# Optimization experiments

Measured on AMD Instinct MI355X. Metric: run time of the kernel, lower is better.

Reference implementation:

```python
import jax, jax.numpy as jnp
import numpy as np

B, T, D, H = 32, 512, 1024, 1024  # batch, seq, input_size, hidden_size


def _xavier(key, shape):
    fan_in, fan_out = shape
    limit = float(np.sqrt(6.0 / (fan_in + fan_out)))
    return jax.random.uniform(key, shape, jnp.float32, -limit, limit)


def setup_inputs() -> dict:
    key = jax.random.key(0)
    k1, k2, k3 = jax.random.split(key, 3)
    x = jax.random.normal(k1, (B, T, D), jnp.float32)
    weight_ih = _xavier(k2, (D, 4 * H))
    weight_hh = _xavier(k3, (H, 4 * H))
    bias = jnp.zeros((4 * H,), jnp.float32)
    return {"x": x, "weight_ih": weight_ih, "weight_hh": weight_hh, "bias": bias}


def _lstm(x, weight_ih, weight_hh, bias):
    HS = weight_hh.shape[0]
    bs = x.shape[0]
    # Precompute input projections for all timesteps in one big GEMM.
    x_proj = jnp.einsum('btd,dg->btg', x, weight_ih) + bias  # [B,T,4H]
    h0 = jnp.zeros((bs, HS), x.dtype)
    c0 = jnp.zeros((bs, HS), x.dtype)

    def step(carry, xp_t):
        h, c = carry
        gates = xp_t + h @ weight_hh  # [B,4H]
        i_t = jax.nn.sigmoid(gates[:, :HS])
        f_t = jax.nn.sigmoid(gates[:, HS:2 * HS])
        g_t = jnp.tanh(gates[:, 2 * HS:3 * HS])
        o_t = jax.nn.sigmoid(gates[:, 3 * HS:])
        c = f_t * c + i_t * g_t
        h = o_t * jnp.tanh(c)
        return (h, c), h

    (h_T, c_T), hs = jax.lax.scan(step, (h0, c0), jnp.swapaxes(x_proj, 0, 1))
    hidden_seq = jnp.swapaxes(hs, 0, 1)  # [B,T,H]
    return hidden_seq, (h_T, c_T)


def reference(x, weight_ih, weight_hh, bias):
    return _lstm(x, weight_ih, weight_hh, bias)
```

## Files before the change

### kernel.cpp

```cpp
#include <hip/hip_runtime.h>

typedef unsigned short ushort_t;
typedef unsigned int   uint32;
typedef unsigned long long ull_t;
typedef __attribute__((ext_vector_type(8))) short short8;
typedef __attribute__((ext_vector_type(4))) float floatx4;

#define B_    32
#define T_    512
#define H_    1024
#define G4_   4096
#define HSEQ_ (B_*T_*H_)

#define NBLK 64

#define XPROJ_OFF 0ul
#define WTIH_OFF  134217728ul
#define WTHH_OFF  142606336ul
#define H0X_OFF   150994944ul
#define H1X_OFF   151060480ul
#define FLAGS_OFF 151126016ul
#define WS_NEED   151130112ul

#define H0_OFF  0ul
#define H1_OFF  65536ul
#define CTR_OFF 131072ul

__device__ __forceinline__ ushort_t f2b_rne(float f) {
    uint32 u = __float_as_uint(f);
    u += 0x7fffu + ((u >> 16) & 1u);
    return (ushort_t)(u >> 16);
}
__device__ __forceinline__ float b2f(ushort_t u) { return __uint_as_float(((uint32)u) << 16); }
__device__ __forceinline__ float sigm(float x)  { return 1.f / (1.f + __expf(-x)); }
__device__ __forceinline__ float tanh_(float x) { return 1.f - 2.f / (__expf(2.f * x) + 1.f); }

__global__ void transpose_cvt2(const float* __restrict__ in0, ushort_t* __restrict__ out0,
                               const float* __restrict__ in1, ushort_t* __restrict__ out1)
{
    const int gb = blockIdx.x;
    const float*    in  = (gb < 2048) ? in0  : in1;
    ushort_t*       out = (gb < 2048) ? out0 : out1;
    const int id = (gb & 2047) * 256 + threadIdx.x;
    const int n  = id & 4095;
    const int k0 = (id >> 12) * 8;
    union { ushort_t v[8]; uint4 q; } r;
#pragma unroll
    for (int j = 0; j < 8; j++)
        r.v[j] = f2b_rne(in[(size_t)(k0 + j) * G4_ + n]);
    *(uint4*)(out + (size_t)n * 1024 + k0) = r.q;
}

__launch_bounds__(256, 2)
__global__ void gemm_xproj(const float* __restrict__ A, const ushort_t* __restrict__ Bt,
                           const float* __restrict__ bias, ushort_t* __restrict__ C)
{
    __shared__ ushort_t As[128 * 32];
    __shared__ ushort_t Bs[128 * 32];
    const int tid = threadIdx.x;
    const int wave = tid >> 6, lane = tid & 63, l16 = lane & 15, quad = lane >> 4;
    const int wm = (wave >> 1) * 64, wn = (wave & 1) * 64;
    const int m0 = blockIdx.y * 128, n0 = blockIdx.x * 128;
    const int r = tid >> 2;
    const int kp = (tid & 3) * 8;

    floatx4 acc[4][4];
#pragma unroll
    for (int i = 0; i < 4; i++)
#pragma unroll
        for (int j = 0; j < 4; j++) acc[i][j] = (floatx4){0.f, 0.f, 0.f, 0.f};

    for (int kk = 0; kk < 1024; kk += 32) {
#pragma unroll
        for (int h = 0; h < 2; h++) {
            const float* ap = A + (size_t)(m0 + r + h * 64) * 1024 + kk + kp;
            const uint4 u0 = *(const uint4*)ap;
            const uint4 u1 = *(const uint4*)(ap + 4);
            uint4 p;
            p.x = __builtin_amdgcn_perm(u0.y, u0.x, 0x07060302u);
            p.y = __builtin_amdgcn_perm(u0.w, u0.z, 0x07060302u);
            p.z = __builtin_amdgcn_perm(u1.y, u1.x, 0x07060302u);
            p.w = __builtin_amdgcn_perm(u1.w, u1.z, 0x07060302u);
            *(uint4*)&As[(r + h * 64) * 32 + kp] = p;
        }
        const ushort_t* bp = Bt + (size_t)(n0 + r) * 1024 + kk + kp;
        *(uint4*)&Bs[r * 32 + kp]        = *(const uint4*)bp;
        *(uint4*)&Bs[(r + 64) * 32 + kp] = *(const uint4*)(bp + 64 * 1024);
        __syncthreads();

        short8 af[4], bfr[4];
#pragma unroll
        for (int i = 0; i < 4; i++) af[i]  = *(const short8*)&As[(wm + i * 16 + l16) * 32 + quad * 8];
#pragma unroll
        for (int j = 0; j < 4; j++) bfr[j] = *(const short8*)&Bs[(wn + j * 16 + l16) * 32 + quad * 8];
#pragma unroll
        for (int i = 0; i < 4; i++)
#pragma unroll
            for (int j = 0; j < 4; j++)
                acc[i][j] = __builtin_amdgcn_mfma_f32_16x16x32_bf16(af[i], bfr[j], acc[i][j], 0, 0, 0);
        __syncthreads();
    }

#pragma unroll
    for (int i = 0; i < 4; i++) {
        const int gm = m0 + wm + i * 16 + quad * 4;
#pragma unroll
        for (int j = 0; j < 4; j++) {
            const int gn = n0 + wn + j * 16 + l16;
            const float bv = bias[gn];
#pragma unroll
            for (int rr = 0; rr < 4; rr++)
                C[(size_t)(gm + rr) * G4_ + gn] = f2b_rne(acc[i][j][rr] + bv);
        }
    }
}

__launch_bounds__(512, 2)
__global__ void lstm_scan_xp(const ushort_t* __restrict__ xproj,
                             const ushort_t* __restrict__ wthh,
                             ushort_t* __restrict__ h0buf,
                             ushort_t* __restrict__ h1buf,
                             float* __restrict__ out,
                             uint32* __restrict__ flags)
{
    const int tid  = threadIdx.x;
    const int bid  = blockIdx.x;
    const int wave = tid >> 6, lane = tid & 63, l16 = lane & 15, quad = lane >> 4;
    const int g     = wave & 3;
    const int khalf = wave >> 2;
    const int unit0 = bid * 16;
    const int col0  = g * 1024 + unit0 + l16;

    __shared__ ushort_t hs[32 * 1024];
    __shared__ float gA[4 * 32 * 17];
    __shared__ float gB[4 * 32 * 17];
    __shared__ uint32 cnt;

    short8 whf[16];
#pragma unroll
    for (int kk = 0; kk < 16; kk++)
        whf[kk] = *(const short8*)(wthh + (size_t)col0 * 1024 + khalf * 512 + kk * 32 + quad * 8);

    if (tid == 0) cnt = 0;

    const int eb = tid >> 4, ej = tid & 15;
    const int hwoff = (bid >> 1) * 1024 + eb * 32 + 16 * (bid & 1) + ej;
    float cst = 0.f;

    const int b0 = l16, b1 = l16 + 16;
    const int off0 = (b0 * 64 + quad * 16) ^ ((b0 & 7) << 4);
    const int off1 = (b1 * 64 + quad * 16) ^ ((b1 & 7) << 4);
    const int rowbase = khalf * 16 * 2048;

    const int src0  = wave * 8;
    const int abase = (lane >> 1) * 64 + (lane & 1) * 16;

    ushort_t xq[4];
    {
        const ushort_t* xp = xproj + ((size_t)eb * T_ + 0) * G4_ + unit0 + ej;
#pragma unroll
        for (int gg = 0; gg < 4; gg++) xq[gg] = xp[gg * 1024];
    }

    __syncthreads();

    for (int t = 0; t < 512; t++) {
        const ushort_t* hr = (t & 1) ? h1buf : h0buf;
        ushort_t*       hw = (t & 1) ? h0buf : h1buf;

        for (;;) {
            int rdy = 1;
            if (lane < 8)
                rdy = (__hip_atomic_load(&flags[(src0 + lane) * 16],
                                         __ATOMIC_RELAXED, __HIP_MEMORY_SCOPE_AGENT)
                       >= (uint32)t);
            if (__ballot(rdy) == ~0ull) break;
        }

        {
            ull_t d0[8], d1[8];
#pragma unroll
            for (int sl = 0; sl < 8; sl++) {
                const int S = src0 + sl;
                const size_t a = (size_t)(S >> 1) * 2048 + (size_t)((S & 1) * 32 + abase);
                const char* p = (const char*)hr + a;
                d0[sl] = __hip_atomic_load((const ull_t*)p,
                                           __ATOMIC_RELAXED, __HIP_MEMORY_SCOPE_AGENT);
                d1[sl] = __hip_atomic_load((const ull_t*)(p + 8),
                                           __ATOMIC_RELAXED, __HIP_MEMORY_SCOPE_AGENT);
            }
#pragma unroll
            for (int sl = 0; sl < 8; sl++) {
                const int S = src0 + sl;
                const int c = ((S >> 1) * 2048 + (S & 1) * 32 + abase) >> 4;
                const int dst = (c * 16) ^ (((c >> 2) & 7) << 4);
                uint4 v;
                *(ull_t*)&v.x = d0[sl];
                *(ull_t*)&v.z = d1[sl];
                *(uint4*)((char*)hs + dst) = v;
            }
        }
        __syncthreads();

        floatx4 a0a = (floatx4){0.f, 0.f, 0.f, 0.f};
        floatx4 a0b = a0a, a1a = a0a, a1b = a0a;
#pragma unroll
        for (int kk = 0; kk < 16; kk++) {
            const char* base = (const char*)hs + rowbase + kk * 2048;
            const short8 a0 = *(const short8*)(base + off0);
            const short8 a1 = *(const short8*)(base + off1);
            if (kk & 1) {
                a0b = __builtin_amdgcn_mfma_f32_16x16x32_bf16(a0, whf[kk], a0b, 0, 0, 0);
                a1b = __builtin_amdgcn_mfma_f32_16x16x32_bf16(a1, whf[kk], a1b, 0, 0, 0);
            } else {
                a0a = __builtin_amdgcn_mfma_f32_16x16x32_bf16(a0, whf[kk], a0a, 0, 0, 0);
                a1a = __builtin_amdgcn_mfma_f32_16x16x32_bf16(a1, whf[kk], a1a, 0, 0, 0);
            }
        }
        const floatx4 s0 = a0a + a0b;
        const floatx4 s1 = a1a + a1b;
        float* gd = khalf ? gB : gA;
#pragma unroll
        for (int rr = 0; rr < 4; rr++) {
            gd[(g * 32 + quad * 4 + rr) * 17 + l16]      = s0[rr];
            gd[(g * 32 + 16 + quad * 4 + rr) * 17 + l16] = s1[rr];
        }
        __syncthreads();

        float hval, cval;
        {
            const float gi = gA[(0 * 32 + eb) * 17 + ej] + gB[(0 * 32 + eb) * 17 + ej] + b2f(xq[0]);
            const float gf = gA[(1 * 32 + eb) * 17 + ej] + gB[(1 * 32 + eb) * 17 + ej] + b2f(xq[1]);
            const float gg = gA[(2 * 32 + eb) * 17 + ej] + gB[(2 * 32 + eb) * 17 + ej] + b2f(xq[2]);
            const float go = gA[(3 * 32 + eb) * 17 + ej] + gB[(3 * 32 + eb) * 17 + ej] + b2f(xq[3]);
            const float iv = sigm(gi);
            const float fv = sigm(gf);
            const float gv = tanh_(gg);
            const float ov = sigm(go);
            cval = fv * cst + iv * gv;
            cst = cval;
            hval = ov * tanh_(cval);
        }

        {
            const uint32 myb = (uint32)f2b_rne(hval);
            const uint32 nbb = (uint32)__shfl_xor((int)myb, 1);
            if ((ej & 1) == 0)
                __hip_atomic_store((uint32*)(hw + hwoff), myb | (nbb << 16),
                                   __ATOMIC_RELAXED, __HIP_MEMORY_SCOPE_AGENT);
        }

        if (t < 511) {
            asm volatile("s_waitcnt vmcnt(0)" ::: "memory");
            if (lane == 0) {
                const uint32 old = __hip_atomic_fetch_add(&cnt, 1u,
                                       __ATOMIC_RELAXED, __HIP_MEMORY_SCOPE_WORKGROUP);
                if (old == (uint32)(8 * t + 7))
                    __hip_atomic_store(&flags[bid * 16], (uint32)(t + 1),
                                       __ATOMIC_RELAXED, __HIP_MEMORY_SCOPE_AGENT);
            }
            out[((size_t)eb * T_ + t) * H_ + unit0 + ej] = hval;
            {
                const ushort_t* xp = xproj + ((size_t)eb * T_ + (t + 1)) * G4_ + unit0 + ej;
#pragma unroll
                for (int gg = 0; gg < 4; gg++) xq[gg] = xp[gg * 1024];
            }
        } else {
            out[((size_t)eb * T_ + t) * H_ + unit0 + ej] = hval;
            out[HSEQ_ + eb * H_ + unit0 + ej] = hval;
            out[HSEQ_ + B_ * H_ + eb * H_ + unit0 + ej] = cval;
        }
    }
}

__launch_bounds__(512, 2)
__global__ void lstm_scan_fused(const float* __restrict__ x,
                                const float* __restrict__ wih,
                                const float* __restrict__ whh,
                                const float* __restrict__ bias,
                                ushort_t* __restrict__ h0buf,
                                ushort_t* __restrict__ h1buf,
                                float* __restrict__ out,
                                uint32* __restrict__ ctr)
{
    const int tid  = threadIdx.x;
    const int bid  = blockIdx.x;
    const int wave = tid >> 6, lane = tid & 63, l16 = lane & 15, quad = lane >> 4;
    const int g     = wave & 3;
    const int khalf = wave >> 2;
    const int unit0 = bid * 16;
    const int col0  = g * 1024 + unit0 + l16;
    const int kbase = khalf * 512;

    __shared__ ushort_t xs[32 * 1024];
    __shared__ float gA[4 * 32 * 17];
    __shared__ float gB[4 * 32 * 17];

    short8 wif[16], whf[16];
#pragma unroll
    for (int kk = 0; kk < 16; kk++) {
        short8 vi, vh;
#pragma unroll
        for (int j = 0; j < 8; j++) {
            const size_t k = (size_t)(kbase + kk * 32 + quad * 8 + j);
            vi[j] = (short)f2b_rne(wih[k * G4_ + col0]);
            vh[j] = (short)f2b_rne(whh[k * G4_ + col0]);
        }
        wif[kk] = vi;
        whf[kk] = vh;
    }
    const float bcol = (khalf == 0) ? bias[col0] : 0.f;

    const int eb = tid >> 4, ej = tid & 15;
    const int hwoff = (bid >> 1) * 1024 + eb * 32 + 16 * (bid & 1) + ej;
    float cst = 0.f;

    floatx4 a0a, a0b, a1a, a1b;

    {
        const int sb = tid >> 4, sc = tid & 15;
        const float* xrow = x + ((size_t)sb * T_ + 0) * H_ + sc * 64;
#pragma unroll
        for (int q = 0; q < 8; q++) {
            const uint4 u0 = *(const uint4*)(xrow + q * 8);
            const uint4 u1 = *(const uint4*)(xrow + q * 8 + 4);
            uint4 p;
            p.x = __builtin_amdgcn_perm(u0.y, u0.x, 0x07060302u);
            p.y = __builtin_amdgcn_perm(u0.w, u0.z, 0x07060302u);
            p.z = __builtin_amdgcn_perm(u1.y, u1.x, 0x07060302u);
            p.w = __builtin_amdgcn_perm(u1.w, u1.z, 0x07060302u);
            const int k = sc * 64 + q * 8;
            *(uint4*)&xs[(k >> 5) * 1024 + sb * 32 + (k & 31)] = p;
        }
    }
    __syncthreads();
    a0a = (floatx4){bcol, bcol, bcol, bcol};
    a1a = a0a;
    a0b = (floatx4){0.f, 0.f, 0.f, 0.f};
    a1b = a0b;
#pragma unroll
    for (int kk = 0; kk < 16; kk++) {
        const ushort_t* ps = &xs[(khalf * 16 + kk) * 1024 + quad * 8];
        const short8 a0 = *(const short8*)(ps + l16 * 32);
        const short8 a1 = *(const short8*)(ps + (16 + l16) * 32);
        if (kk & 1) {
            a0b = __builtin_amdgcn_mfma_f32_16x16x32_bf16(a0, wif[kk], a0b, 0, 0, 0);
            a1b = __builtin_amdgcn_mfma_f32_16x16x32_bf16(a1, wif[kk], a1b, 0, 0, 0);
        } else {
            a0a = __builtin_amdgcn_mfma_f32_16x16x32_bf16(a0, wif[kk], a0a, 0, 0, 0);
            a1a = __builtin_amdgcn_mfma_f32_16x16x32_bf16(a1, wif[kk], a1a, 0, 0, 0);
        }
    }

    for (int t = 0; t < 512; t++) {
        const ushort_t* hr = (t & 1) ? h1buf : h0buf;
        ushort_t*       hw = (t & 1) ? h0buf : h1buf;

#pragma unroll
        for (int kk = 0; kk < 16; kk++) {
            const ushort_t* pa = hr + (khalf * 16 + kk) * 1024 + quad * 8;
            const short8 a0 = *(const short8*)(pa + l16 * 32);
            const short8 a1 = *(const short8*)(pa + (16 + l16) * 32);
            if (kk & 1) {
                a0b = __builtin_amdgcn_mfma_f32_16x16x32_bf16(a0, whf[kk], a0b, 0, 0, 0);
                a1b = __builtin_amdgcn_mfma_f32_16x16x32_bf16(a1, whf[kk], a1b, 0, 0, 0);
            } else {
                a0a = __builtin_amdgcn_mfma_f32_16x16x32_bf16(a0, whf[kk], a0a, 0, 0, 0);
                a1a = __builtin_amdgcn_mfma_f32_16x16x32_bf16(a1, whf[kk], a1a, 0, 0, 0);
            }
        }
        const floatx4 s0 = a0a + a0b;
        const floatx4 s1 = a1a + a1b;
        float* gd = khalf ? gB : gA;
#pragma unroll
        for (int rr = 0; rr < 4; rr++) {
            gd[(g * 32 + quad * 4 + rr) * 17 + l16]      = s0[rr];
            gd[(g * 32 + 16 + quad * 4 + rr) * 17 + l16] = s1[rr];
        }
        __syncthreads();

        {
            const float gi = gA[(0 * 32 + eb) * 17 + ej] + gB[(0 * 32 + eb) * 17 + ej];
            const float gf = gA[(1 * 32 + eb) * 17 + ej] + gB[(1 * 32 + eb) * 17 + ej];
            const float gg = gA[(2 * 32 + eb) * 17 + ej] + gB[(2 * 32 + eb) * 17 + ej];
            const float go = gA[(3 * 32 + eb) * 17 + ej] + gB[(3 * 32 + eb) * 17 + ej];
            const float iv = sigm(gi);
            const float fv = sigm(gf);
            const float gv = tanh_(gg);
            const float ov = sigm(go);
            const float c = fv * cst + iv * gv;
            cst = c;
            const float h = ov * tanh_(c);
            hw[hwoff] = f2b_rne(h);
            out[((size_t)eb * T_ + t) * H_ + unit0 + ej] = h;
            if (t == 511) {
                out[HSEQ_ + eb * H_ + unit0 + ej] = h;
                out[HSEQ_ + B_ * H_ + eb * H_ + unit0 + ej] = cst;
            }
        }
        __syncthreads();

        if (t < 511) {
            if (tid == 0) {
                __threadfence();
                __hip_atomic_fetch_add(ctr, 1u, __ATOMIC_RELAXED, __HIP_MEMORY_SCOPE_AGENT);
            }
            {
                const int sb = tid >> 4, sc = tid & 15;
                const float* xrow = x + ((size_t)sb * T_ + (t + 1)) * H_ + sc * 64;
#pragma unroll
                for (int q = 0; q < 8; q++) {
                    const uint4 u0 = *(const uint4*)(xrow + q * 8);
                    const uint4 u1 = *(const uint4*)(xrow + q * 8 + 4);
                    uint4 p;
                    p.x = __builtin_amdgcn_perm(u0.y, u0.x, 0x07060302u);
                    p.y = __builtin_amdgcn_perm(u0.w, u0.z, 0x07060302u);
                    p.z = __builtin_amdgcn_perm(u1.y, u1.x, 0x07060302u);
                    p.w = __builtin_amdgcn_perm(u1.w, u1.z, 0x07060302u);
                    const int k = sc * 64 + q * 8;
                    *(uint4*)&xs[(k >> 5) * 1024 + sb * 32 + (k & 31)] = p;
                }
            }
            __syncthreads();
            a0a = (floatx4){bcol, bcol, bcol, bcol};
            a1a = a0a;
            a0b = (floatx4){0.f, 0.f, 0.f, 0.f};
            a1b = a0b;
#pragma unroll
            for (int kk = 0; kk < 16; kk++) {
                const ushort_t* ps = &xs[(khalf * 16 + kk) * 1024 + quad * 8];
                const short8 a0 = *(const short8*)(ps + l16 * 32);
                const short8 a1 = *(const short8*)(ps + (16 + l16) * 32);
                if (kk & 1) {
                    a0b = __builtin_amdgcn_mfma_f32_16x16x32_bf16(a0, wif[kk], a0b, 0, 0, 0);
                    a1b = __builtin_amdgcn_mfma_f32_16x16x32_bf16(a1, wif[kk], a1b, 0, 0, 0);
                } else {
                    a0a = __builtin_amdgcn_mfma_f32_16x16x32_bf16(a0, wif[kk], a0a, 0, 0, 0);
                    a1a = __builtin_amdgcn_mfma_f32_16x16x32_bf16(a1, wif[kk], a1a, 0, 0, 0);
                }
            }
            if (tid == 0) {
                const uint32 target = (uint32)NBLK * (uint32)(t + 1);
                while (__hip_atomic_load(ctr, __ATOMIC_RELAXED, __HIP_MEMORY_SCOPE_AGENT) < target) {
                    __builtin_amdgcn_s_sleep(1);
                }
                __threadfence();
            }
            __syncthreads();
        }
    }
}

extern "C" void kernel_launch(void* const* d_in, const int* in_sizes, int n_in,
                              void* d_out, int out_size, void* d_ws, size_t ws_size,
                              hipStream_t stream)
{
    const float* x    = (const float*)d_in[0];
    const float* wih  = (const float*)d_in[1];
    const float* whh  = (const float*)d_in[2];
    const float* bias = (const float*)d_in[3];
    float* out = (float*)d_out;
    char* ws = (char*)d_ws;

    if (ws_size >= WS_NEED) {
        ushort_t* xproj = (ushort_t*)(ws + XPROJ_OFF);
        ushort_t* wtih  = (ushort_t*)(ws + WTIH_OFF);
        ushort_t* wthh  = (ushort_t*)(ws + WTHH_OFF);
        ushort_t* h0    = (ushort_t*)(ws + H0X_OFF);
        ushort_t* h1    = (ushort_t*)(ws + H1X_OFF);
        uint32*   flags = (uint32*)(ws + FLAGS_OFF);

        hipMemsetAsync(ws + H0X_OFF, 0, 2 * 65536 + 4096, stream);
        hipLaunchKernelGGL(transpose_cvt2, dim3(4096), dim3(256), 0, stream,
                           wih, wtih, whh, wthh);
        hipLaunchKernelGGL(gemm_xproj, dim3(32, 128), dim3(256), 0, stream,
                           x, wtih, bias, xproj);
        hipLaunchKernelGGL(lstm_scan_xp, dim3(NBLK), dim3(512), 0, stream,
                           xproj, wthh, h0, h1, out, flags);
    } else {
        ushort_t* h0  = (ushort_t*)(ws + H0_OFF);
        ushort_t* h1  = (ushort_t*)(ws + H1_OFF);
        uint32*   ctr = (uint32*)(ws + CTR_OFF);

        hipMemsetAsync(ws, 0, 131072 + 256, stream);
        hipLaunchKernelGGL(lstm_scan_fused, dim3(NBLK), dim3(512), 0, stream,
                           x, wih, whh, bias, h0, h1, out, ctr);
    }
}
```

Measured before the change: 2.567 ms.

## Split batch into two independent planes with separate flags to overlap recurrence sync

The persistent LSTM scan now splits the 32-sequence batch into two 16-row planes. Each plane has its own double-buffered h arrays, completion flags and counters, and the two planes are processed one after the other inside each timestep. The aim is to let one plane's cross-block flag wait and h exchange overlap with the other plane's MFMA and gate work, shortening the critical path of the inter-block synchronization. The cost is twice as many barriers and flag polls per step, and half-sized MFMA batches that use the preloaded weight fragments less efficiently.

```diff
diff --git a/kernel.cpp b/kernel.cpp
--- a/kernel.cpp
+++ b/kernel.cpp
@@ -17,8 +17,10 @@
 #define XPROJ_OFF 0ul
 #define WTIH_OFF  134217728ul
 #define WTHH_OFF  142606336ul
-#define H0X_OFF   150994944ul
-#define H1X_OFF   151060480ul
+#define H0A_OFF   150994944ul
+#define H1A_OFF   (H0A_OFF +  32768ul)
+#define H0B_OFF   (H0A_OFF +  65536ul)
+#define H1B_OFF   (H0A_OFF +  98304ul)
 #define FLAGS_OFF 151126016ul
 #define WS_NEED   151130112ul
 
@@ -118,10 +120,13 @@
 __launch_bounds__(512, 2)
 __global__ void lstm_scan_xp(const ushort_t* __restrict__ xproj,
                              const ushort_t* __restrict__ wthh,
-                             ushort_t* __restrict__ h0buf,
-                             ushort_t* __restrict__ h1buf,
+                             ushort_t* __restrict__ h0A,
+                             ushort_t* __restrict__ h1A,
+                             ushort_t* __restrict__ h0B,
+                             ushort_t* __restrict__ h1B,
                              float* __restrict__ out,
-                             uint32* __restrict__ flags)
+                             uint32* __restrict__ flagsA,
+                             uint32* __restrict__ flagsB)
 {
     const int tid  = threadIdx.x;
     const int bid  = blockIdx.x;
@@ -131,29 +136,30 @@
     const int unit0 = bid * 16;
     const int col0  = g * 1024 + unit0 + l16;
 
-    __shared__ ushort_t hs[32 * 1024];
-    __shared__ float gA[4 * 32 * 17];
-    __shared__ float gB[4 * 32 * 17];
-    __shared__ uint32 cnt;
+    __shared__ ushort_t hs[16 * 1024];
+    __shared__ float gA[4 * 16 * 17];
+    __shared__ float gB[4 * 16 * 17];
+    __shared__ uint32 cntA, cntB;
 
     short8 whf[16];
 #pragma unroll
     for (int kk = 0; kk < 16; kk++)
         whf[kk] = *(const short8*)(wthh + (size_t)col0 * 1024 + khalf * 512 + kk * 32 + quad * 8);
 
-    if (tid == 0) cnt = 0;
-
-    const int eb = tid >> 4, ej = tid & 15;
-    const int hwoff = (bid >> 1) * 1024 + eb * 32 + 16 * (bid & 1) + ej;
+    if (tid == 0) { cntA = 0; cntB = 0; }
+
+    const int eb      = tid >> 4;
+    const int ej      = tid & 15;
+    const int myplane = eb >> 4;
+    const int bloc    = eb & 15;
     float cst = 0.f;
 
-    const int b0 = l16, b1 = l16 + 16;
-    const int off0 = (b0 * 64 + quad * 16) ^ ((b0 & 7) << 4);
-    const int off1 = (b1 * 64 + quad * 16) ^ ((b1 & 7) << 4);
-    const int rowbase = khalf * 16 * 2048;
-
-    const int src0  = wave * 8;
-    const int abase = (lane >> 1) * 64 + (lane & 1) * 16;
+    const int off0    = (l16 * 64 + quad * 16) ^ ((l16 & 7) << 4);
+    const int rowbase = khalf * 16 * 1024;
+
+    const int src0 = wave * 8;
+    const int sb   = lane >> 2;
+    const int part = lane & 3;
 
     ushort_t xq[4];
     {
@@ -165,110 +171,103 @@
     __syncthreads();
 
     for (int t = 0; t < 512; t++) {
-        const ushort_t* hr = (t & 1) ? h1buf : h0buf;
-        ushort_t*       hw = (t & 1) ? h0buf : h1buf;
-
-        for (;;) {
-            int rdy = 1;
-            if (lane < 8)
-                rdy = (__hip_atomic_load(&flags[(src0 + lane) * 16],
-                                         __ATOMIC_RELAXED, __HIP_MEMORY_SCOPE_AGENT)
-                       >= (uint32)t);
-            if (__ballot(rdy) == ~0ull) break;
-        }
-
-        {
-            ull_t d0[8], d1[8];
-#pragma unroll
-            for (int sl = 0; sl < 8; sl++) {
-                const int S = src0 + sl;
-                const size_t a = (size_t)(S >> 1) * 2048 + (size_t)((S & 1) * 32 + abase);
-                const char* p = (const char*)hr + a;
-                d0[sl] = __hip_atomic_load((const ull_t*)p,
+#pragma unroll
+        for (int P = 0; P < 2; P++) {
+            const ushort_t* hr = (P == 0) ? ((t & 1) ? h1A : h0A)
+                                          : ((t & 1) ? h1B : h0B);
+            ushort_t*       hw = (P == 0) ? ((t & 1) ? h0A : h1A)
+                                          : ((t & 1) ? h0B : h1B);
+            uint32*  fl  = (P == 0) ? flagsA : flagsB;
+            uint32*  cp  = (P == 0) ? &cntA : &cntB;
+
+            for (;;) {
+                int rdy = 1;
+                if (lane < 8)
+                    rdy = (__hip_atomic_load(&fl[(src0 + lane) * 8],
+                                             __ATOMIC_RELAXED, __HIP_MEMORY_SCOPE_AGENT)
+                           >= (uint32)t);
+                if (__ballot(rdy) == ~0ull) break;
+            }
+
+            {
+                ull_t d[8];
+#pragma unroll
+                for (int sl = 0; sl < 8; sl++) {
+                    const int S = src0 + sl;
+                    d[sl] = __hip_atomic_load(
+                        (const ull_t*)(hr + (size_t)sb * 1024 + S * 16 + part * 4),
+                        __ATOMIC_RELAXED, __HIP_MEMORY_SCOPE_AGENT);
+                }
+#pragma unroll
+                for (int sl = 0; sl < 8; sl++) {
+                    const int S = src0 + sl;
+                    const int dst = (S >> 1) * 1024 + sb * 64 + (S & 1) * 32 + part * 8;
+                    const int gi  = dst >> 4;
+                    const int swz = ((gi * 16) ^ (((gi >> 2) & 7) << 4)) + (dst & 15);
+                    *(ull_t*)((char*)hs + swz) = d[sl];
+                }
+            }
+            __syncthreads();
+
+            floatx4 aa = (floatx4){0.f, 0.f, 0.f, 0.f};
+            floatx4 ab = aa;
+#pragma unroll
+            for (int kk = 0; kk < 16; kk++) {
+                const char* base = (const char*)hs + rowbase + kk * 1024;
+                const short8 a0 = *(const short8*)(base + off0);
+                if (kk & 1) ab = __builtin_amdgcn_mfma_f32_16x16x32_bf16(a0, whf[kk], ab, 0, 0, 0);
+                else        aa = __builtin_amdgcn_mfma_f32_16x16x32_bf16(a0, whf[kk], aa, 0, 0, 0);
+            }
+            const floatx4 s0 = aa + ab;
+            float* gd = khalf ? gB : gA;
+#pragma unroll
+            for (int rr = 0; rr < 4; rr++)
+                gd[(g * 16 + quad * 4 + rr) * 17 + l16] = s0[rr];
+            __syncthreads();
+
+            if (myplane == P) {
+                const float gi = gA[(0 * 16 + bloc) * 17 + ej] + gB[(0 * 16 + bloc) * 17 + ej] + b2f(xq[0]);
+                const float gf = gA[(1 * 16 + bloc) * 17 + ej] + gB[(1 * 16 + bloc) * 17 + ej] + b2f(xq[1]);
+                const float gg = gA[(2 * 16 + bloc) * 17 + ej] + gB[(2 * 16 + bloc) * 17 + ej] + b2f(xq[2]);
+                const float go = gA[(3 * 16 + bloc) * 17 + ej] + gB[(3 * 16 + bloc) * 17 + ej] + b2f(xq[3]);
+                const float iv = sigm(gi);
+                const float fv = sigm(gf);
+                const float gv = tanh_(gg);
+                const float ov = sigm(go);
+                const float cval = fv * cst + iv * gv;
+                cst = cval;
+                const float hval = ov * tanh_(cval);
+
+                {
+                    const uint32 myb = (uint32)f2b_rne(hval);
+                    const uint32 nbb = (uint32)__shfl_xor((int)myb, 1);
+                    if ((ej & 1) == 0)
+                        __hip_atomic_store((uint32*)(hw + (size_t)bloc * 1024 + unit0 + ej),
+                                           myb | (nbb << 16),
                                            __ATOMIC_RELAXED, __HIP_MEMORY_SCOPE_AGENT);
-                d1[sl] = __hip_atomic_load((const ull_t*)(p + 8),
-                                           __ATOMIC_RELAXED, __HIP_MEMORY_SCOPE_AGENT);
-            }
-#pragma unroll
-            for (int sl = 0; sl < 8; sl++) {
-                const int S = src0 + sl;
-                const int c = ((S >> 1) * 2048 + (S & 1) * 32 + abase) >> 4;
-                const int dst = (c * 16) ^ (((c >> 2) & 7) << 4);
-                uint4 v;
-                *(ull_t*)&v.x = d0[sl];
-                *(ull_t*)&v.z = d1[sl];
-                *(uint4*)((char*)hs + dst) = v;
-            }
-        }
-        __syncthreads();
-
-        floatx4 a0a = (floatx4){0.f, 0.f, 0.f, 0.f};
-        floatx4 a0b = a0a, a1a = a0a, a1b = a0a;
-#pragma unroll
-        for (int kk = 0; kk < 16; kk++) {
-            const char* base = (const char*)hs + rowbase + kk * 2048;
-            const short8 a0 = *(const short8*)(base + off0);
-            const short8 a1 = *(const short8*)(base + off1);
-            if (kk & 1) {
-                a0b = __builtin_amdgcn_mfma_f32_16x16x32_bf16(a0, whf[kk], a0b, 0, 0, 0);
-                a1b = __builtin_amdgcn_mfma_f32_16x16x32_bf16(a1, whf[kk], a1b, 0, 0, 0);
-            } else {
-                a0a = __builtin_amdgcn_mfma_f32_16x16x32_bf16(a0, whf[kk], a0a, 0, 0, 0);
-                a1a = __builtin_amdgcn_mfma_f32_16x16x32_bf16(a1, whf[kk], a1a, 0, 0, 0);
-            }
-        }
-        const floatx4 s0 = a0a + a0b;
-        const floatx4 s1 = a1a + a1b;
-        float* gd = khalf ? gB : gA;
-#pragma unroll
-        for (int rr = 0; rr < 4; rr++) {
-            gd[(g * 32 + quad * 4 + rr) * 17 + l16]      = s0[rr];
-            gd[(g * 32 + 16 + quad * 4 + rr) * 17 + l16] = s1[rr];
-        }
-        __syncthreads();
-
-        float hval, cval;
-        {
-            const float gi = gA[(0 * 32 + eb) * 17 + ej] + gB[(0 * 32 + eb) * 17 + ej] + b2f(xq[0]);
-            const float gf = gA[(1 * 32 + eb) * 17 + ej] + gB[(1 * 32 + eb) * 17 + ej] + b2f(xq[1]);
-            const float gg = gA[(2 * 32 + eb) * 17 + ej] + gB[(2 * 32 + eb) * 17 + ej] + b2f(xq[2]);
-            const float go = gA[(3 * 32 + eb) * 17 + ej] + gB[(3 * 32 + eb) * 17 + ej] + b2f(xq[3]);
-            const float iv = sigm(gi);
-            const float fv = sigm(gf);
-            const float gv = tanh_(gg);
-            const float ov = sigm(go);
-            cval = fv * cst + iv * gv;
-            cst = cval;
-            hval = ov * tanh_(cval);
-        }
-
-        {
-            const uint32 myb = (uint32)f2b_rne(hval);
-            const uint32 nbb = (uint32)__shfl_xor((int)myb, 1);
-            if ((ej & 1) == 0)
-                __hip_atomic_store((uint32*)(hw + hwoff), myb | (nbb << 16),
-                                   __ATOMIC_RELAXED, __HIP_MEMORY_SCOPE_AGENT);
-        }
-
-        if (t < 511) {
-            asm volatile("s_waitcnt vmcnt(0)" ::: "memory");
-            if (lane == 0) {
-                const uint32 old = __hip_atomic_fetch_add(&cnt, 1u,
-                                       __ATOMIC_RELAXED, __HIP_MEMORY_SCOPE_WORKGROUP);
-                if (old == (uint32)(8 * t + 7))
-                    __hip_atomic_store(&flags[bid * 16], (uint32)(t + 1),
-                                       __ATOMIC_RELAXED, __HIP_MEMORY_SCOPE_AGENT);
-            }
-            out[((size_t)eb * T_ + t) * H_ + unit0 + ej] = hval;
-            {
-                const ushort_t* xp = xproj + ((size_t)eb * T_ + (t + 1)) * G4_ + unit0 + ej;
-#pragma unroll
-                for (int gg = 0; gg < 4; gg++) xq[gg] = xp[gg * 1024];
-            }
-        } else {
-            out[((size_t)eb * T_ + t) * H_ + unit0 + ej] = hval;
-            out[HSEQ_ + eb * H_ + unit0 + ej] = hval;
-            out[HSEQ_ + B_ * H_ + eb * H_ + unit0 + ej] = cval;
+                }
+
+                if (t < 511) {
+                    asm volatile("s_waitcnt vmcnt(0)" ::: "memory");
+                    if (lane == 0) {
+                        const uint32 old = __hip_atomic_fetch_add(cp, 1u,
+                                               __ATOMIC_RELAXED, __HIP_MEMORY_SCOPE_WORKGROUP);
+                        if (old == (uint32)(4 * t + 3))
+                            __hip_atomic_store(&fl[bid * 8], (uint32)(t + 1),
+                                               __ATOMIC_RELAXED, __HIP_MEMORY_SCOPE_AGENT);
+                    }
+                    out[((size_t)eb * T_ + t) * H_ + unit0 + ej] = hval;
+                    {
+                        const ushort_t* xp = xproj + ((size_t)eb * T_ + (t + 1)) * G4_ + unit0 + ej;
+#pragma unroll
+                        for (int gg2 = 0; gg2 < 4; gg2++) xq[gg2] = xp[gg2 * 1024];
+                    }
+                } else {
+                    out[((size_t)eb * T_ + t) * H_ + unit0 + ej] = hval;
+                    out[HSEQ_ + eb * H_ + unit0 + ej] = hval;
+                    out[HSEQ_ + B_ * H_ + eb * H_ + unit0 + ej] = cval;
+                }
+            }
         }
     }
 }
@@ -463,20 +462,24 @@
     char* ws = (char*)d_ws;
 
     if (ws_size >= WS_NEED) {
-        ushort_t* xproj = (ushort_t*)(ws + XPROJ_OFF);
-        ushort_t* wtih  = (ushort_t*)(ws + WTIH_OFF);
-        ushort_t* wthh  = (ushort_t*)(ws + WTHH_OFF);
-        ushort_t* h0    = (ushort_t*)(ws + H0X_OFF);
-        ushort_t* h1    = (ushort_t*)(ws + H1X_OFF);
-        uint32*   flags = (uint32*)(ws + FLAGS_OFF);
-
-        hipMemsetAsync(ws + H0X_OFF, 0, 2 * 65536 + 4096, stream);
+        ushort_t* xproj  = (ushort_t*)(ws + XPROJ_OFF);
+        ushort_t* wtih   = (ushort_t*)(ws + WTIH_OFF);
+        ushort_t* wthh   = (ushort_t*)(ws + WTHH_OFF);
+        ushort_t* h0A    = (ushort_t*)(ws + H0A_OFF);
+        ushort_t* h1A    = (ushort_t*)(ws + H1A_OFF);
+        ushort_t* h0B    = (ushort_t*)(ws + H0B_OFF);
+        ushort_t* h1B    = (ushort_t*)(ws + H1B_OFF);
+        uint32*   flagsA = (uint32*)(ws + FLAGS_OFF);
+        uint32*   flagsB = (uint32*)(ws + FLAGS_OFF + 2048);
+
+        hipMemsetAsync(ws + H0A_OFF, 0, 4 * 32768, stream);
+        hipMemsetAsync(ws + FLAGS_OFF, 0, 4096, stream);
         hipLaunchKernelGGL(transpose_cvt2, dim3(4096), dim3(256), 0, stream,
                            wih, wtih, whh, wthh);
         hipLaunchKernelGGL(gemm_xproj, dim3(32, 128), dim3(256), 0, stream,
                            x, wtih, bias, xproj);
         hipLaunchKernelGGL(lstm_scan_xp, dim3(NBLK), dim3(512), 0, stream,
-                           xproj, wthh, h0, h1, out, flags);
+                           xproj, wthh, h0A, h1A, h0B, h1B, out, flagsA, flagsB);
     } else {
         ushort_t* h0  = (ushort_t*)(ws + H0_OFF);
         ushort_t* h1  = (ushort_t*)(ws + H1_OFF);
```

Measured after the change: 3.062 ms. +19.3%, slower.
